# Performance work log

Measured on AMD Instinct MI355X. Metric: run time of the kernel, lower is better.

The kernel has to match this reference:

```python
import jax, jax.numpy as jnp
from jax import lax
import numpy as np

N_BASIS = 256
N_FREQ = 128
N_TIME = 8
LAM = 0.2
LR = 1e-3
B1, B2, EPS = 0.9, 0.999, 1e-8
CONV_TOL = 1e-3


def setup_inputs() -> dict:
    key = jax.random.key(0)
    k1, k2 = jax.random.split(key)
    spec = jax.random.normal(k1, (32, N_FREQ, 256), dtype=jnp.float32)
    basis = jax.random.normal(k2, (N_FREQ * N_TIME, N_BASIS), dtype=jnp.float32)
    return {"spec": spec, "basis": basis, "n_iter_coef": 30, "pad": 0, "stride": 4}


def normalize01(x):
    # torch normalize01 with dims=-1, keepdims
    xmin = x.min(axis=-1, keepdims=True)
    xmax = x.max(axis=-1, keepdims=True)
    return (x - xmin) / (xmax - xmin)


def _response(x, basis, n_iter):
    # x: [B, D]; Adam-optimize coef [B, N_BASIS] for n_iter steps with the
    # same early-stop rule as the torch code (frozen via a done flag).
    B = x.shape[0]
    sig = jnp.std(x, ddof=1)  # torch .std() is unbiased over all elements

    def loss_fn(coef):
        pred = coef @ basis.T                      # [B, D]
        mse = jnp.mean((pred - x) ** 2)
        return mse + LAM * sig * jnp.mean(jnp.abs(coef / sig))

    coef0 = jnp.full((B, N_BASIS), 0.5 / N_BASIS, dtype=jnp.float32)
    m0 = jnp.zeros_like(coef0)
    v0 = jnp.zeros_like(coef0)

    def body(carry, _):
        coef, m, v, t, old_loss, done = carry
        loss, g = jax.value_and_grad(loss_fn)(coef)
        t_new = t + 1.0
        m_new = B1 * m + (1.0 - B1) * g
        v_new = B2 * v + (1.0 - B2) * g * g
        mhat = m_new / (1.0 - B1 ** t_new)
        vhat = v_new / (1.0 - B2 ** t_new)
        coef_new = coef - LR * mhat / (jnp.sqrt(vhat) + EPS)
        conv = jnp.abs(old_loss - loss) / old_loss < CONV_TOL
        sel = lambda a, b: jnp.where(done, a, b)
        new_carry = (
            sel(coef, coef_new),
            sel(m, m_new),
            sel(v, v_new),
            jnp.where(done, t, t_new),
            jnp.where(done, old_loss, loss),
            done | conv,
        )
        return new_carry, None

    init = (coef0, m0, v0, jnp.float32(0.0), jnp.float32(1e-10), jnp.array(False))
    (coef, _, _, _, _, _), _ = lax.scan(body, init, None, length=n_iter)
    return coef  # detached in torch


def reference(spec, basis, n_iter_coef, pad, stride):
    if spec.ndim == 2:
        spec = spec[None, ...]
    B, F, T = spec.shape
    spec_ = jnp.pad(spec, ((0, 0), (0, 0), (pad, pad)))
    starts = np.arange(0, T - N_TIME + 1, stride)          # window start frames
    idx = starts[:, None] + np.arange(N_TIME)              # [W, N_TIME]
    wins = spec_[:, :, idx]                                # [B, F, W, N_TIME]
    x = jnp.transpose(wins, (2, 0, 1, 3)).reshape(len(starts), B, F * N_TIME)
    x = normalize01(x)                                     # per row of [B, D]
    coef = jax.vmap(lambda xw: _response(xw, basis, n_iter_coef))(x)  # [W, B, N_BASIS]
    return jnp.transpose(coef, (1, 2, 0))                  # [B, N_BASIS, W]
```

## Files before the change

kernel.cpp:

```cpp
#include <hip/hip_runtime.h>
#include <math.h>

#define NB     256
#define NF     128
#define FT     1024
#define NW     63
#define TORIG  256
#define MAXIT  48
#define RPB    8
#define NBLK   4
#define GRID   256

__device__ __forceinline__ float rl(float v, int lane) {
    return __uint_as_float((unsigned)__builtin_amdgcn_readlane((int)__float_as_uint(v), lane));
}

__device__ __forceinline__ int xidx(int k2, int cg, int row) {
    return (k2 * 512 + row * 64 + (cg ^ row)) * 4;
}

__global__ __launch_bounds__(512, 2) void window_kernel(
    const float* __restrict__ spec,
    const float* __restrict__ basis,
    float* __restrict__ G,
    const int* __restrict__ p_niter,
    const int* __restrict__ p_pad,
    const int* __restrict__ p_stride,
    double* __restrict__ sxbuf,
    double* __restrict__ gpart,
    unsigned int* __restrict__ gcnt,
    float* __restrict__ out)
{
    __shared__ float  s_p0[RPB * 2048];
    __shared__ float  s_p1[RPB * 2048];
    __shared__ float  s_gred[2][NB];
    __shared__ float  s_mn[RPB], s_rng[RPB];
    __shared__ double s_dred[8];
    __shared__ float  s_redq[2][8], s_redr[2][8];
    __shared__ unsigned int s_wcnt[2];
    __shared__ int    s_stop[2];
    float* const s_xn = s_p1;

    const int bid = blockIdx.x;
    const int yy  = bid >> 3;
    const int q   = yy & 3;
    const int w   = (bid & 7) + 8 * (yy >> 2);
    const int tid = threadIdx.x;
    const int ks  = tid >> 6;
    const int kg  = tid & 63;
    const int r   = kg >> 3;
    const int cgo = 8 * ks + (kg & 7);
    const int n_iter = p_niter[0];
    const int t0     = w * p_stride[0] - p_pad[0];
    unsigned int* gbar = gcnt + MAXIT * NW;

    {
        const int c = tid & 255, jh = tid >> 8;
        float acc = 0.f;
        const float* bp = basis + (size_t)(jh * 512) * NB;
        #pragma unroll 16
        for (int j = 0; j < 512; ++j)
            acc = fmaf(bp[j * NB + bid], bp[j * NB + c], acc);
        s_gred[jh][c] = acc;
        __syncthreads();
        if (jh == 0) G[(size_t)bid * NB + c] = s_gred[0][c] + s_gred[1][c];
    }
    __threadfence();
    __syncthreads();
    if (tid == 0) atomicAdd(gbar, 1u);
    if (w >= NW) return;

    #pragma unroll
    for (int i = 0; i < 16; ++i) {
        const int e = i * 512 + tid;
        const int b = e >> 10, jj = e & 1023;
        const int f = jj >> 3, t = jj & 7, tq = t0 + t;
        s_xn[b * FT + jj] = (tq >= 0 && tq < TORIG)
            ? spec[((size_t)(q * RPB + b) * NF + f) * TORIG + tq] : 0.f;
    }
    __syncthreads();
    {
        float mn = __builtin_inff(), mx = -__builtin_inff();
        #pragma unroll
        for (int i = 0; i < 16; ++i) {
            const float v = s_xn[ks * FT + i * 64 + kg];
            mn = fminf(mn, v); mx = fmaxf(mx, v);
        }
        #pragma unroll
        for (int off = 32; off; off >>= 1) {
            mn = fminf(mn, __shfl_down(mn, off));
            mx = fmaxf(mx, __shfl_down(mx, off));
        }
        if (kg == 0) { s_mn[ks] = mn; s_rng[ks] = mx - mn; }
    }
    __syncthreads();
    double sx2p = 0.0;
    #pragma unroll
    for (int i = 0; i < 16; ++i) {
        const int e = i * 512 + tid;
        const int b = e >> 10, jj = e & 1023;
        const float v = (s_xn[b * FT + jj] - s_mn[b]) / s_rng[b];
        s_xn[b * FT + jj] = v;
        sx2p += (double)v * (double)v;
    }
    #pragma unroll
    for (int off = 32; off; off >>= 1) sx2p += __shfl_down(sx2p, off);
    if (kg == 0) s_dred[ks] = sx2p;
    __syncthreads();
    if (tid == 0) {
        double s = 0.0;
        #pragma unroll
        for (int i = 0; i < 8; ++i) s += s_dred[i];
        sxbuf[w * NBLK + q] = s;
        __threadfence();
    }

    float xbp[RPB][4];
    #pragma unroll
    for (int b = 0; b < RPB; ++b)
        #pragma unroll
        for (int j = 0; j < 4; ++j) xbp[b][j] = 0.f;
    for (int i0 = 0; i0 < 128; i0 += 4) {
        const int jj = ks * 128 + i0;
        float4 bv[4];
        #pragma unroll
        for (int t = 0; t < 4; ++t)
            bv[t] = *(const float4*)(basis + (size_t)(jj + t) * NB + 4 * kg);
        #pragma unroll
        for (int b = 0; b < RPB; ++b) {
            const float4 x4 = *(const float4*)&s_xn[b * FT + jj];
            xbp[b][0] = fmaf(x4.x, bv[0].x, fmaf(x4.y, bv[1].x, fmaf(x4.z, bv[2].x, fmaf(x4.w, bv[3].x, xbp[b][0]))));
            xbp[b][1] = fmaf(x4.x, bv[0].y, fmaf(x4.y, bv[1].y, fmaf(x4.z, bv[2].y, fmaf(x4.w, bv[3].y, xbp[b][1]))));
            xbp[b][2] = fmaf(x4.x, bv[0].z, fmaf(x4.y, bv[1].z, fmaf(x4.z, bv[2].z, fmaf(x4.w, bv[3].z, xbp[b][2]))));
            xbp[b][3] = fmaf(x4.x, bv[0].w, fmaf(x4.y, bv[1].w, fmaf(x4.z, bv[2].w, fmaf(x4.w, bv[3].w, xbp[b][3]))));
        }
    }
    __syncthreads();
    #pragma unroll
    for (int b = 0; b < RPB; ++b)
        *(float4*)&s_p0[xidx(ks, kg, b)] =
            make_float4(xbp[b][0], xbp[b][1], xbp[b][2], xbp[b][3]);
    __syncthreads();
    float xB[4] = {0.f, 0.f, 0.f, 0.f};
    #pragma unroll
    for (int k2 = 0; k2 < 8; ++k2) {
        const float4 p4 = *(const float4*)&s_p0[xidx(k2, cgo, r)];
        xB[0] += p4.x; xB[1] += p4.y; xB[2] += p4.z; xB[3] += p4.w;
    }

    if (tid == 0) {
        while (__hip_atomic_load(gbar, __ATOMIC_ACQUIRE, __HIP_MEMORY_SCOPE_AGENT) < (unsigned)GRID)
            __builtin_amdgcn_s_sleep(1);
    }
    if (tid == 64) { s_wcnt[0] = 0; s_wcnt[1] = 0; s_stop[0] = 0; s_stop[1] = 0; }
    __syncthreads();
    float4 g[32];
    #pragma unroll
    for (int kl = 0; kl < 32; ++kl)
        g[kl] = *(const float4*)(G + (size_t)(32 * ks + kl) * NB + 4 * kg);

    const float C0 = 0.5f / 256.f;
    float cf[4]  = {C0, C0, C0, C0}, cfp[4] = {C0, C0, C0, C0};
    float m_[4]  = {0, 0, 0, 0},    v_[4]  = {0, 0, 0, 0};
    float b1p = 1.f, b2p = 1.f;
    float old_loss = 1e-10f;
    double sxtot = 0.0;
    const float c1 = 2.f / 32768.f, c2 = 0.2f / 8192.f;
    int use_prev = 0;

    for (int it = 0; it < n_iter; ++it) {
        const int p = it & 1;
        float* const sp = p ? s_p1 : s_p0;

        #pragma unroll
        for (int b = 0; b < RPB; ++b) {
            float p0 = 0.f, p1 = 0.f, p2 = 0.f, p3 = 0.f;
            #pragma unroll
            for (int m = 0; m < 8; ++m) {
                const float4 ga = g[4 * m + 0], gb = g[4 * m + 1];
                const float4 gc = g[4 * m + 2], gd = g[4 * m + 3];
                const int L = b * 8 + m;
                const float cx = rl(cf[0], L), cy = rl(cf[1], L);
                const float cz = rl(cf[2], L), cw = rl(cf[3], L);
                p0 = fmaf(cx, ga.x, fmaf(cy, gb.x, fmaf(cz, gc.x, fmaf(cw, gd.x, p0))));
                p1 = fmaf(cx, ga.y, fmaf(cy, gb.y, fmaf(cz, gc.y, fmaf(cw, gd.y, p1))));
                p2 = fmaf(cx, ga.z, fmaf(cy, gb.z, fmaf(cz, gc.z, fmaf(cw, gd.z, p2))));
                p3 = fmaf(cx, ga.w, fmaf(cy, gb.w, fmaf(cz, gc.w, fmaf(cw, gd.w, p3))));
            }
            *(float4*)&sp[xidx(ks, kg, b)] = make_float4(p0, p1, p2, p3);
        }

        if (tid == 64 && it >= 2) {
            const int itc = it - 2;
            while (__hip_atomic_load(&gcnt[itc * NW + w], __ATOMIC_ACQUIRE,
                                     __HIP_MEMORY_SCOPE_AGENT) < (unsigned)NBLK)
                __builtin_amdgcn_s_sleep(1);
            const size_t pbm = ((size_t)itc * NW + w) * NBLK;
            double Qt = 0.0, Rt = 0.0;
            #pragma unroll
            for (int i = 0; i < NBLK; ++i) {
                Qt += gpart[(pbm + i) * 2 + 0];
                Rt += gpart[(pbm + i) * 2 + 1];
            }
            if (itc == 0)
                sxtot = sxbuf[w * NBLK + 0] + sxbuf[w * NBLK + 1] +
                        sxbuf[w * NBLK + 2] + sxbuf[w * NBLK + 3];
            const float loss = (float)((Qt + sxtot) / 32768.0 + 0.2 * (Rt / 8192.0));
            const float stat = fabsf(old_loss - loss) / old_loss;
            old_loss = loss;
            s_stop[p] = (stat < 1e-3f) ? 1 : 0;
        }

        __syncthreads();

        if (s_stop[p]) { use_prev = 1; break; }

        float a4[4] = {0.f, 0.f, 0.f, 0.f};
        #pragma unroll
        for (int k2 = 0; k2 < 8; ++k2) {
            const float4 p4 = *(const float4*)&sp[xidx(k2, cgo, r)];
            a4[0] += p4.x; a4[1] += p4.y; a4[2] += p4.z; a4[3] += p4.w;
        }

        if (it + 1 < n_iter) {
            float qc = 0.f, rr = 0.f;
            #pragma unroll
            for (int j = 0; j < 4; ++j) {
                qc += cf[j] * (a4[j] - 2.f * xB[j]);
                rr += fabsf(cf[j]);
            }
            #pragma unroll
            for (int off = 32; off; off >>= 1) {
                qc += __shfl_down(qc, off);
                rr += __shfl_down(rr, off);
            }
            if (kg == 0) {
                s_redq[p][ks] = qc; s_redr[p][ks] = rr;
                __threadfence_block();
                const unsigned old = __hip_atomic_fetch_add(&s_wcnt[p], 1u,
                                        __ATOMIC_ACQ_REL, __HIP_MEMORY_SCOPE_WORKGROUP);
                if (old == 7u) {
                    float Q = 0.f, R = 0.f;
                    #pragma unroll
                    for (int i = 0; i < 8; ++i) { Q += s_redq[p][i]; R += s_redr[p][i]; }
                    s_wcnt[p] = 0u;
                    const size_t pb = ((size_t)it * NW + w) * NBLK;
                    gpart[(pb + q) * 2 + 0] = (double)Q;
                    gpart[(pb + q) * 2 + 1] = (double)R;
                    __hip_atomic_fetch_add(&gcnt[it * NW + w], 1u,
                                           __ATOMIC_RELEASE, __HIP_MEMORY_SCOPE_AGENT);
                }
            }
        }

        b1p *= 0.9f; b2p *= 0.999f;
        const float rb1 = __builtin_amdgcn_rcpf(1.f - b1p);
        const float rb2 = __builtin_amdgcn_rcpf(1.f - b2p);
        #pragma unroll
        for (int j = 0; j < 4; ++j) {
            const float c_ = cf[j];
            cfp[j] = c_;
            const float sgn = (c_ > 0.f) ? 1.f : ((c_ < 0.f) ? -1.f : 0.f);
            const float gg = c1 * (a4[j] - xB[j]) + c2 * sgn;
            m_[j] = 0.9f * m_[j] + 0.1f * gg;
            v_[j] = 0.999f * v_[j] + 0.001f * gg * gg;
            const float den = __builtin_amdgcn_sqrtf(v_[j] * rb2) + 1e-8f;
            cf[j] = c_ - 1e-3f * (m_[j] * rb1) * __builtin_amdgcn_rcpf(den);
        }
    }

    if (!use_prev && n_iter >= 2) {
        if (tid == 64) {
            const int itc = n_iter - 2;
            while (__hip_atomic_load(&gcnt[itc * NW + w], __ATOMIC_ACQUIRE,
                                     __HIP_MEMORY_SCOPE_AGENT) < (unsigned)NBLK)
                __builtin_amdgcn_s_sleep(1);
            const size_t pbm = ((size_t)itc * NW + w) * NBLK;
            double Qt = 0.0, Rt = 0.0;
            #pragma unroll
            for (int i = 0; i < NBLK; ++i) {
                Qt += gpart[(pbm + i) * 2 + 0];
                Rt += gpart[(pbm + i) * 2 + 1];
            }
            if (itc == 0)
                sxtot = sxbuf[w * NBLK + 0] + sxbuf[w * NBLK + 1] +
                        sxbuf[w * NBLK + 2] + sxbuf[w * NBLK + 3];
            const float loss = (float)((Qt + sxtot) / 32768.0 + 0.2 * (Rt / 8192.0));
            const float stat = fabsf(old_loss - loss) / old_loss;
            s_stop[0] = (stat < 1e-3f) ? 1 : 0;
        }
        __syncthreads();
        use_prev = s_stop[0];
    }

    #pragma unroll
    for (int j = 0; j < 4; ++j)
        out[((size_t)(q * RPB + r) * NB + 4 * cgo + j) * NW + w] =
            use_prev ? cfp[j] : cf[j];
}

extern "C" void kernel_launch(void* const* d_in, const int* in_sizes, int n_in,
                              void* d_out, int out_size, void* d_ws, size_t ws_size,
                              hipStream_t stream)
{
    const float* spec   = (const float*)d_in[0];
    const float* basis  = (const float*)d_in[1];
    const int* p_niter  = (const int*)d_in[2];
    const int* p_pad    = (const int*)d_in[3];
    const int* p_stride = (const int*)d_in[4];
    float* out = (float*)d_out;

    char* ws = (char*)d_ws;
    float*        G     = (float*)ws;
    double*       sxbuf = (double*)(ws + 262144);
    double*       gpart = (double*)(ws + 266240);
    unsigned int* gcnt  = (unsigned int*)(ws + 266240 + 193536);

    hipMemsetAsync(gcnt, 0, (MAXIT * NW + 1) * sizeof(unsigned int), stream);
    window_kernel<<<dim3(GRID), dim3(512), 0, stream>>>(
        spec, basis, G, p_niter, p_pad, p_stride, sxbuf, gpart, gcnt, out);
}
```

Measured before the change: 284.2 us.

## Compute per-iteration Gram product with split-bf16 MFMA instead of FP32 FMAs

```diff
diff --git a/kernel.cpp b/kernel.cpp
--- a/kernel.cpp
+++ b/kernel.cpp
@@ -11,12 +11,16 @@
 #define NBLK   4
 #define GRID   256
 
-__device__ __forceinline__ float rl(float v, int lane) {
-    return __uint_as_float((unsigned)__builtin_amdgcn_readlane((int)__float_as_uint(v), lane));
-}
+using f32x4  = __attribute__((ext_vector_type(4))) float;
+using bf16x8 = __attribute__((ext_vector_type(8))) short;
 
 __device__ __forceinline__ int xidx(int k2, int cg, int row) {
     return (k2 * 512 + row * 64 + (cg ^ row)) * 4;
+}
+
+__device__ __forceinline__ unsigned bf16_hi(float x) {
+    const unsigned u = __float_as_uint(x);
+    return (u + 0x7fffu + ((u >> 16) & 1u)) >> 16;
 }
 
 __global__ __launch_bounds__(512, 2) void window_kernel(
@@ -31,15 +35,16 @@
     unsigned int* __restrict__ gcnt,
     float* __restrict__ out)
 {
-    __shared__ float  s_p0[RPB * 2048];
-    __shared__ float  s_p1[RPB * 2048];
+    __shared__ __align__(16) float s_p0[RPB * 2048];
+    __shared__ __align__(16) float s_xn[RPB * FT];
+    __shared__ __align__(16) short A0[16 * NB];
+    __shared__ __align__(16) short A1[16 * NB];
     __shared__ float  s_gred[2][NB];
     __shared__ float  s_mn[RPB], s_rng[RPB];
     __shared__ double s_dred[8];
     __shared__ float  s_redq[2][8], s_redr[2][8];
     __shared__ unsigned int s_wcnt[2];
     __shared__ int    s_stop[2];
-    float* const s_xn = s_p1;
 
     const int bid = blockIdx.x;
     const int yy  = bid >> 3;
@@ -141,12 +146,13 @@
         *(float4*)&s_p0[xidx(ks, kg, b)] =
             make_float4(xbp[b][0], xbp[b][1], xbp[b][2], xbp[b][3]);
     __syncthreads();
-    float xB[4] = {0.f, 0.f, 0.f, 0.f};
+    float xBo[4] = {0.f, 0.f, 0.f, 0.f};
     #pragma unroll
     for (int k2 = 0; k2 < 8; ++k2) {
         const float4 p4 = *(const float4*)&s_p0[xidx(k2, cgo, r)];
-        xB[0] += p4.x; xB[1] += p4.y; xB[2] += p4.z; xB[3] += p4.w;
-    }
+        xBo[0] += p4.x; xBo[1] += p4.y; xBo[2] += p4.z; xBo[3] += p4.w;
+    }
+    *(float4*)&s_xn[r * NB + 4 * cgo] = make_float4(xBo[0], xBo[1], xBo[2], xBo[3]);
 
     if (tid == 0) {
         while (__hip_atomic_load(gbar, __ATOMIC_ACQUIRE, __HIP_MEMORY_SCOPE_AGENT) < (unsigned)GRID)
@@ -154,41 +160,91 @@
     }
     if (tid == 64) { s_wcnt[0] = 0; s_wcnt[1] = 0; s_stop[0] = 0; s_stop[1] = 0; }
     __syncthreads();
-    float4 g[32];
-    #pragma unroll
-    for (int kl = 0; kl < 32; ++kl)
-        g[kl] = *(const float4*)(G + (size_t)(32 * ks + kl) * NB + 4 * kg);
+
+    const int lr  = kg & 15;
+    const int lh  = kg >> 4;
+    const int hlf = kg >> 5;
+
+    float xB[8];
+    #pragma unroll
+    for (int T = 0; T < 2; ++T)
+        #pragma unroll
+        for (int t = 0; t < 4; ++t)
+            xB[4*T + t] = s_xn[(4*(lh & 1) + t) * NB + 32*ks + 16*T + lr];
+
+    bf16x8 Gh[8][2], Gl[8][2];
+    {
+        const float* gp = G + (size_t)(8 * lh) * NB + 32 * ks + lr;
+        #pragma unroll
+        for (int kk = 0; kk < 8; ++kk)
+            #pragma unroll
+            for (int T = 0; T < 2; ++T)
+                #pragma unroll
+                for (int b = 0; b < 8; ++b) {
+                    const float gv = gp[(size_t)(32*kk + b) * NB + 16*T];
+                    const unsigned hb = bf16_hi(gv);
+                    const float    hf = __uint_as_float(hb << 16);
+                    const unsigned lb = bf16_hi(gv - hf);
+                    Gh[kk][T][b] = (short)hb;
+                    Gl[kk][T][b] = (short)lb;
+                }
+    }
+
+    unsigned awaddr[8];
+    #pragma unroll
+    for (int T = 0; T < 2; ++T)
+        #pragma unroll
+        for (int t = 0; t < 4; ++t) {
+            const int hr  = 4*(lh & 1) + t;
+            const int col = 32*ks + 16*T + lr;
+            awaddr[4*T + t] = (unsigned)((((hr * NB + col) ^ ((hr & 7) << 3)) * 2)
+                                         + (hlf ? 4096 : 0));
+        }
+    const unsigned abase = (unsigned)(((lr * NB + lh * 8) ^ ((lr & 7) << 3)) * 2);
 
     const float C0 = 0.5f / 256.f;
-    float cf[4]  = {C0, C0, C0, C0}, cfp[4] = {C0, C0, C0, C0};
-    float m_[4]  = {0, 0, 0, 0},    v_[4]  = {0, 0, 0, 0};
+    float cf[8], cfp[8], m_[8], v_[8];
+    #pragma unroll
+    for (int j = 0; j < 8; ++j) { cf[j] = C0; cfp[j] = C0; m_[j] = 0.f; v_[j] = 0.f; }
+    {
+        const short vh  = (short)bf16_hi(C0);
+        const short val = hlf ? (short)0 : vh;
+        #pragma unroll
+        for (int j = 0; j < 8; ++j)
+            *(short*)((char*)A0 + awaddr[j]) = val;
+    }
     float b1p = 1.f, b2p = 1.f;
     float old_loss = 1e-10f;
     double sxtot = 0.0;
-    const float c1 = 2.f / 32768.f, c2 = 0.2f / 8192.f;
+    const float c1c = 2.f / 32768.f, c2c = 0.2f / 8192.f;
     int use_prev = 0;
 
     for (int it = 0; it < n_iter; ++it) {
         const int p = it & 1;
-        float* const sp = p ? s_p1 : s_p0;
-
-        #pragma unroll
-        for (int b = 0; b < RPB; ++b) {
-            float p0 = 0.f, p1 = 0.f, p2 = 0.f, p3 = 0.f;
-            #pragma unroll
-            for (int m = 0; m < 8; ++m) {
-                const float4 ga = g[4 * m + 0], gb = g[4 * m + 1];
-                const float4 gc = g[4 * m + 2], gd = g[4 * m + 3];
-                const int L = b * 8 + m;
-                const float cx = rl(cf[0], L), cy = rl(cf[1], L);
-                const float cz = rl(cf[2], L), cw = rl(cf[3], L);
-                p0 = fmaf(cx, ga.x, fmaf(cy, gb.x, fmaf(cz, gc.x, fmaf(cw, gd.x, p0))));
-                p1 = fmaf(cx, ga.y, fmaf(cy, gb.y, fmaf(cz, gc.y, fmaf(cw, gd.y, p1))));
-                p2 = fmaf(cx, ga.z, fmaf(cy, gb.z, fmaf(cz, gc.z, fmaf(cw, gd.z, p2))));
-                p3 = fmaf(cx, ga.w, fmaf(cy, gb.w, fmaf(cz, gc.w, fmaf(cw, gd.w, p3))));
-            }
-            *(float4*)&sp[xidx(ks, kg, b)] = make_float4(p0, p1, p2, p3);
-        }
+        const char* rdb = (const char*)(p ? A1 : A0);
+        char*       wrb = (char*)(p ? A0 : A1);
+
+        __syncthreads();
+
+        f32x4 a1[2], a2[2];
+        const f32x4 z4 = {0.f, 0.f, 0.f, 0.f};
+        a1[0] = z4; a1[1] = z4; a2[0] = z4; a2[1] = z4;
+        #pragma unroll
+        for (int kk = 0; kk < 8; ++kk) {
+            const bf16x8 af = *(const bf16x8*)(rdb + (abase ^ (unsigned)(kk << 6)));
+            a1[0] = __builtin_amdgcn_mfma_f32_16x16x32_bf16(af, Gh[kk][0], a1[0], 0, 0, 0);
+            a2[0] = __builtin_amdgcn_mfma_f32_16x16x32_bf16(af, Gl[kk][0], a2[0], 0, 0, 0);
+            a1[1] = __builtin_amdgcn_mfma_f32_16x16x32_bf16(af, Gh[kk][1], a1[1], 0, 0, 0);
+            a2[1] = __builtin_amdgcn_mfma_f32_16x16x32_bf16(af, Gl[kk][1], a2[1], 0, 0, 0);
+        }
+        float a4[8];
+        #pragma unroll
+        for (int T = 0; T < 2; ++T)
+            #pragma unroll
+            for (int t = 0; t < 4; ++t) {
+                const float s = a1[T][t] + a2[T][t];
+                a4[4*T + t] = s + __shfl_xor(s, 32);
+            }
 
         if (tid == 64 && it >= 2) {
             const int itc = it - 2;
@@ -215,20 +271,14 @@
 
         if (s_stop[p]) { use_prev = 1; break; }
 
-        float a4[4] = {0.f, 0.f, 0.f, 0.f};
-        #pragma unroll
-        for (int k2 = 0; k2 < 8; ++k2) {
-            const float4 p4 = *(const float4*)&sp[xidx(k2, cgo, r)];
-            a4[0] += p4.x; a4[1] += p4.y; a4[2] += p4.z; a4[3] += p4.w;
-        }
-
         if (it + 1 < n_iter) {
             float qc = 0.f, rr = 0.f;
             #pragma unroll
-            for (int j = 0; j < 4; ++j) {
+            for (int j = 0; j < 8; ++j) {
                 qc += cf[j] * (a4[j] - 2.f * xB[j]);
                 rr += fabsf(cf[j]);
             }
+            if (kg >= 32) { qc = 0.f; rr = 0.f; }
             #pragma unroll
             for (int off = 32; off; off >>= 1) {
                 qc += __shfl_down(qc, off);
@@ -257,15 +307,23 @@
         const float rb1 = __builtin_amdgcn_rcpf(1.f - b1p);
         const float rb2 = __builtin_amdgcn_rcpf(1.f - b2p);
         #pragma unroll
-        for (int j = 0; j < 4; ++j) {
+        for (int j = 0; j < 8; ++j) {
             const float c_ = cf[j];
             cfp[j] = c_;
             const float sgn = (c_ > 0.f) ? 1.f : ((c_ < 0.f) ? -1.f : 0.f);
-            const float gg = c1 * (a4[j] - xB[j]) + c2 * sgn;
+            const float gg = c1c * (a4[j] - xB[j]) + c2c * sgn;
             m_[j] = 0.9f * m_[j] + 0.1f * gg;
             v_[j] = 0.999f * v_[j] + 0.001f * gg * gg;
             const float den = __builtin_amdgcn_sqrtf(v_[j] * rb2) + 1e-8f;
             cf[j] = c_ - 1e-3f * (m_[j] * rb1) * __builtin_amdgcn_rcpf(den);
+        }
+
+        #pragma unroll
+        for (int j = 0; j < 8; ++j) {
+            const unsigned hb = bf16_hi(cf[j]);
+            const float    hf = __uint_as_float(hb << 16);
+            const unsigned lb = bf16_hi(cf[j] - hf);
+            *(short*)(wrb + awaddr[j]) = (short)(hlf ? lb : hb);
         }
     }
 
@@ -293,10 +351,14 @@
         use_prev = s_stop[0];
     }
 
-    #pragma unroll
-    for (int j = 0; j < 4; ++j)
-        out[((size_t)(q * RPB + r) * NB + 4 * cgo + j) * NW + w] =
-            use_prev ? cfp[j] : cf[j];
+    if (kg < 32) {
+        #pragma unroll
+        for (int T = 0; T < 2; ++T)
+            #pragma unroll
+            for (int t = 0; t < 4; ++t)
+                out[((size_t)(q * RPB + 4*lh + t) * NB + 32*ks + 16*T + lr) * NW + w] =
+                    use_prev ? cfp[4*T + t] : cf[4*T + t];
+    }
 }
 
 extern "C" void kernel_launch(void* const* d_in, const int* in_sizes, int n_in,
```

Result: slower. 291.2 us (+2.5%).
